# Optimization experiments

Measured on AMD Instinct MI355X. Metric: run time of the kernel, lower is better.

The kernel has to match this reference:

```python
import jax, jax.numpy as jnp
import numpy as np

S, D, H, DK, DV = 4096, 1024, 16, 64, 64


def setup_inputs() -> dict:
    key = jax.random.key(0)
    ks = jax.random.split(key, 6)
    x = jax.random.normal(ks[0], (S, D), dtype=jnp.float32)
    # per-head projection weights, stacked over heads; scaled for numerical sanity
    Wq = jax.random.normal(ks[1], (H, D, DK), dtype=jnp.float32) / np.sqrt(D)
    Wk = jax.random.normal(ks[2], (H, D, DK), dtype=jnp.float32) / np.sqrt(D)
    Wv = jax.random.normal(ks[3], (H, D, DV), dtype=jnp.float32) / np.sqrt(D)
    Wc = jax.random.normal(ks[4], (H * DV, D), dtype=jnp.float32) / np.sqrt(H * DV)
    bc = jnp.zeros((D,), dtype=jnp.float32)
    return {"x": x, "Wq": Wq, "Wk": Wk, "Wv": Wv, "Wc": Wc, "bc": bc}


def reference(x, Wq, Wk, Wv, Wc, bc):
    # Per-head projections (original loops over heads with separate Linears;
    # stacking over h is the same math, vectorized).
    q = jnp.einsum("sd,hdk->hsk", x, Wq)   # [H,S,DK]
    k = jnp.einsum("sd,hdk->hsk", x, Wk)   # [H,S,DK]
    v = jnp.einsum("sd,hdv->hsv", x, Wv)   # [H,S,DV]
    scores = jnp.einsum("hsk,htk->hst", q, k) / jnp.sqrt(jnp.asarray(DK, x.dtype))
    probs = jax.nn.softmax(scores, axis=-1)  # softmax over last dim, per row
    o = jnp.einsum("hst,htv->hsv", probs, v)  # [H,S,DV]
    cat = jnp.transpose(o, (1, 0, 2)).reshape(S, H * DV)  # concat heads on last dim
    return cat @ Wc + bc  # output projection with bias
```

## Files before the change

kernel.cpp:

```cpp
#include <hip/hip_runtime.h>
#include <hip/hip_bf16.h>

#define S_ 4096
#define D_ 1024
#define H_ 16
#define DK_ 64
#define DV_ 64

typedef short bf16x8 __attribute__((ext_vector_type(8)));
typedef float floatx4 __attribute__((ext_vector_type(4)));
using bf16 = __hip_bfloat16;

#define MFMA16(a, b, c) __builtin_amdgcn_mfma_f32_16x16x32_bf16(a, b, c, 0, 0, 0)

__device__ __forceinline__ void stage16(const void* g, void* l) {
    __builtin_amdgcn_global_load_lds(
        (const __attribute__((address_space(1))) void*)g,
        (__attribute__((address_space(3))) void*)l, 16, 0, 0);
}

__device__ __forceinline__ bf16x8 ldsfrag(const bf16* base, int row, int chunk) {
    return *(const bf16x8*)(base + row * 64 + ((chunk ^ (row & 7)) << 3));
}

__global__ __launch_bounds__(256)
void cvt_x(const float* __restrict__ x, bf16* __restrict__ xb)
{
    int i = (blockIdx.x * 256 + threadIdx.x) * 8;
    float4 a = *(const float4*)(x + i);
    float4 b = *(const float4*)(x + i + 4);
    union { bf16x8 v; bf16 e[8]; } u;
    u.e[0] = __float2bfloat16(a.x); u.e[1] = __float2bfloat16(a.y);
    u.e[2] = __float2bfloat16(a.z); u.e[3] = __float2bfloat16(a.w);
    u.e[4] = __float2bfloat16(b.x); u.e[5] = __float2bfloat16(b.y);
    u.e[6] = __float2bfloat16(b.z); u.e[7] = __float2bfloat16(b.w);
    *(bf16x8*)(xb + i) = u.v;
}

__global__ __launch_bounds__(256)
void transpose_cvt(const float* __restrict__ src, bf16* __restrict__ dst,
                   int R, int C, long srcMatStride, long dstMatStride, float scale)
{
    const float* s = src + (size_t)blockIdx.z * srcMatStride;
    bf16* d = dst + (size_t)blockIdx.z * dstMatStride;
    int r0 = blockIdx.x * 64, c0 = blockIdx.y * 64;
    __shared__ float ls[64][65];
    int t = threadIdx.x;
    {
        int r = t >> 2, cseg = (t & 3) * 16;
        const float* sp = s + (size_t)(r0 + r) * C + c0 + cseg;
        #pragma unroll
        for (int i = 0; i < 16; i += 4) {
            float4 v = *(const float4*)(sp + i);
            ls[r][cseg + i + 0] = v.x; ls[r][cseg + i + 1] = v.y;
            ls[r][cseg + i + 2] = v.z; ls[r][cseg + i + 3] = v.w;
        }
    }
    __syncthreads();
    {
        int c = t >> 2, rseg = (t & 3) * 16;
        bf16* dp = d + (size_t)(c0 + c) * R + r0 + rseg;
        #pragma unroll
        for (int i = 0; i < 16; i++) dp[i] = __float2bfloat16(ls[rseg + i][c] * scale);
    }
}

__global__ __launch_bounds__(256)
void qkv_gemm(const bf16* __restrict__ xb, const bf16* __restrict__ Wt,
              bf16* __restrict__ Qb, bf16* __restrict__ Kb, bf16* __restrict__ Vtb)
{
    const int m0 = blockIdx.x * 128;
    const int h  = blockIdx.y;
    __shared__ __align__(16) bf16 xa[2][128 * 64];
    __shared__ __align__(16) bf16 wb[2][192 * 64];

    const int t = threadIdx.x, lane = t & 63, w = t >> 6;
    const int l15 = lane & 15, quad = lane >> 4;

    auto stage_x = [&](int buf, int kk) {
        #pragma unroll
        for (int j = 0; j < 4; j++) {
            int c = (j * 4 + w) * 64 + lane;
            int row = c >> 3, ch = (c & 7) ^ (row & 7);
            stage16((const char*)(xb + (size_t)(m0 + row) * D_ + kk) + ch * 16,
                    (char*)&xa[buf][0] + (j * 4 + w) * 1024);
        }
    };
    auto stage_w = [&](int buf, int kk) {
        #pragma unroll
        for (int j = 0; j < 6; j++) {
            int c = (j * 4 + w) * 64 + lane;
            int row = c >> 3, ch = (c & 7) ^ (row & 7);
            const bf16* g = Wt + (size_t)(row >> 6) * (H_ * 64 * 1024)
                               + (size_t)h * (64 * 1024)
                               + (size_t)(row & 63) * 1024 + kk;
            stage16((const char*)g + ch * 16, (char*)&wb[buf][0] + (j * 4 + w) * 1024);
        }
    };

    const floatx4 fz = {0.f, 0.f, 0.f, 0.f};
    floatx4 acc[2][12];
    #pragma unroll
    for (int mt = 0; mt < 2; mt++)
        #pragma unroll
        for (int nt = 0; nt < 12; nt++) acc[mt][nt] = fz;

    stage_x(0, 0); stage_w(0, 0);
    for (int kt = 0; kt < 16; kt++) {
        int cur = kt & 1;
        __syncthreads();
        if (kt < 15) { stage_x(cur ^ 1, (kt + 1) * 64); stage_w(cur ^ 1, (kt + 1) * 64); }
        #pragma unroll
        for (int ks = 0; ks < 2; ks++) {
            bf16x8 a0 = ldsfrag(&xa[cur][0], w * 32 + l15,      ks * 4 + quad);
            bf16x8 a1 = ldsfrag(&xa[cur][0], w * 32 + 16 + l15, ks * 4 + quad);
            #pragma unroll
            for (int nt = 0; nt < 12; nt++) {
                bf16x8 b = ldsfrag(&wb[cur][0], nt * 16 + l15, ks * 4 + quad);
                acc[0][nt] = MFMA16(a0, b, acc[0][nt]);
                acc[1][nt] = MFMA16(a1, b, acc[1][nt]);
            }
        }
    }

    #pragma unroll
    for (int nt = 0; nt < 12; nt++) {
        int which = nt >> 2;
        int col = (nt & 3) * 16 + l15;
        #pragma unroll
        for (int mt = 0; mt < 2; mt++)
            #pragma unroll
            for (int r = 0; r < 4; r++) {
                int s = m0 + w * 32 + mt * 16 + quad * 4 + r;
                bf16 val = __float2bfloat16(acc[mt][nt][r]);
                if (which == 0)      Qb[((size_t)h * S_ + s) * 64 + col] = val;
                else if (which == 1) Kb[((size_t)h * S_ + s) * 64 + col] = val;
                else                 Vtb[((size_t)h * 64 + col) * S_ + s] = val;
            }
    }
}

__global__ __launch_bounds__(256)
void attn(const bf16* __restrict__ Qb, const bf16* __restrict__ Kb,
          const bf16* __restrict__ Vtb, bf16* __restrict__ Cat)
{
    const int m0 = blockIdx.x * 128;
    const int h  = blockIdx.y;
    __shared__ __align__(16) bf16 ka[2][64 * 64];
    __shared__ __align__(16) bf16 vt[2][64 * 64];
    __shared__ __align__(16) bf16 pl[128 * 72];

    const int t = threadIdx.x, lane = t & 63, w = t >> 6;
    const int l15 = lane & 15, quad = lane >> 4;

    auto stage_kv = [&](int buf, int key0) {
        const char* kg = (const char*)(Kb + ((size_t)h * S_ + key0) * 64);
        #pragma unroll
        for (int j = 0; j < 2; j++) {
            int c = (j * 4 + w) * 64 + lane;
            int row = c >> 3, ch = (c & 7) ^ (row & 7);
            stage16(kg + row * 128 + ch * 16, (char*)&ka[buf][0] + (j * 4 + w) * 1024);
        }
        const char* vg = (const char*)(Vtb + (size_t)h * 64 * S_ + key0);
        #pragma unroll
        for (int j = 0; j < 2; j++) {
            int c = (j * 4 + w) * 64 + lane;
            int row = c >> 3, ch = (c & 7) ^ (row & 7);
            stage16(vg + (size_t)row * (S_ * 2) + ch * 16, (char*)&vt[buf][0] + (j * 4 + w) * 1024);
        }
    };

    {
        const char* qg = (const char*)(Qb + ((size_t)h * S_ + m0) * 64);
        #pragma unroll
        for (int j = 0; j < 4; j++) {
            int c = (j * 4 + w) * 64 + lane;
            int row = c >> 3, ch = (c & 7) ^ (row & 7);
            stage16(qg + row * 128 + ch * 16, (char*)pl + (j * 4 + w) * 1024);
        }
    }
    stage_kv(0, 0);
    __syncthreads();

    bf16x8 qf[2][2];
    #pragma unroll
    for (int mt = 0; mt < 2; mt++)
        #pragma unroll
        for (int ks = 0; ks < 2; ks++)
            qf[mt][ks] = ldsfrag((const bf16*)pl, w * 32 + mt * 16 + l15, ks * 4 + quad);
    __syncthreads();

    const floatx4 fz = {0.f, 0.f, 0.f, 0.f};
    floatx4 acc[2][4];
    float rs[2][4];
    #pragma unroll
    for (int mt = 0; mt < 2; mt++) {
        #pragma unroll
        for (int nt = 0; nt < 4; nt++) acc[mt][nt] = fz;
        #pragma unroll
        for (int r = 0; r < 4; r++) rs[mt][r] = 0.f;
    }

    for (int kt = 0; kt < S_ / 64; kt++) {
        const int cur = kt & 1;
        if (kt + 1 < S_ / 64) stage_kv(cur ^ 1, (kt + 1) * 64);

        floatx4 sc[2][4];
        #pragma unroll
        for (int mt = 0; mt < 2; mt++)
            #pragma unroll
            for (int nt = 0; nt < 4; nt++) sc[mt][nt] = fz;
        #pragma unroll
        for (int ks = 0; ks < 2; ks++) {
            #pragma unroll
            for (int nt = 0; nt < 4; nt++) {
                bf16x8 b = ldsfrag(&ka[cur][0], nt * 16 + l15, ks * 4 + quad);
                sc[0][nt] = MFMA16(qf[0][ks], b, sc[0][nt]);
                sc[1][nt] = MFMA16(qf[1][ks], b, sc[1][nt]);
            }
        }

        #pragma unroll
        for (int mt = 0; mt < 2; mt++)
            #pragma unroll
            for (int nt = 0; nt < 4; nt++)
                #pragma unroll
                for (int r = 0; r < 4; r++) {
                    float p = __expf(sc[mt][nt][r]);
                    rs[mt][r] += p;
                    pl[(w * 32 + mt * 16 + quad * 4 + r) * 72 + nt * 16 + l15] =
                        __float2bfloat16(p);
                }
        asm volatile("s_waitcnt lgkmcnt(0)" ::: "memory");

        #pragma unroll
        for (int ks = 0; ks < 2; ks++) {
            bf16x8 a0 = *(const bf16x8*)(pl + (w * 32 + l15) * 72 + ks * 32 + quad * 8);
            bf16x8 a1 = *(const bf16x8*)(pl + (w * 32 + 16 + l15) * 72 + ks * 32 + quad * 8);
            #pragma unroll
            for (int nt = 0; nt < 4; nt++) {
                bf16x8 b = ldsfrag(&vt[cur][0], nt * 16 + l15, ks * 4 + quad);
                acc[0][nt] = MFMA16(a0, b, acc[0][nt]);
                acc[1][nt] = MFMA16(a1, b, acc[1][nt]);
            }
        }
        __syncthreads();
    }

    #pragma unroll
    for (int mt = 0; mt < 2; mt++)
        #pragma unroll
        for (int r = 0; r < 4; r++) {
            float s_ = rs[mt][r];
            s_ += __shfl_xor(s_, 1, 16);
            s_ += __shfl_xor(s_, 2, 16);
            s_ += __shfl_xor(s_, 4, 16);
            s_ += __shfl_xor(s_, 8, 16);
            float inv = 1.0f / s_;
            int srow = m0 + w * 32 + mt * 16 + quad * 4 + r;
            #pragma unroll
            for (int nt = 0; nt < 4; nt++)
                Cat[(size_t)srow * (H_ * DV_) + h * 64 + nt * 16 + l15] =
                    __float2bfloat16(acc[mt][nt][r] * inv);
        }
}

__global__ __launch_bounds__(256)
void out_proj(const bf16* __restrict__ Cat, const bf16* __restrict__ Wct,
              const float* __restrict__ bc, float* __restrict__ out)
{
    const int m0 = blockIdx.x * 128;
    const int n0 = blockIdx.y * 128;
    __shared__ __align__(16) bf16 ca[2][128 * 64];
    __shared__ __align__(16) bf16 wb[2][128 * 64];

    const int t = threadIdx.x, lane = t & 63, w = t >> 6;
    const int l15 = lane & 15, quad = lane >> 4;

    auto stage_a = [&](int buf, int kk) {
        #pragma unroll
        for (int j = 0; j < 4; j++) {
            int c = (j * 4 + w) * 64 + lane;
            int row = c >> 3, ch = (c & 7) ^ (row & 7);
            stage16((const char*)(Cat + (size_t)(m0 + row) * D_ + kk) + ch * 16,
                    (char*)&ca[buf][0] + (j * 4 + w) * 1024);
        }
    };
    auto stage_b = [&](int buf, int kk) {
        #pragma unroll
        for (int j = 0; j < 4; j++) {
            int c = (j * 4 + w) * 64 + lane;
            int row = c >> 3, ch = (c & 7) ^ (row & 7);
            stage16((const char*)(Wct + (size_t)(n0 + row) * D_ + kk) + ch * 16,
                    (char*)&wb[buf][0] + (j * 4 + w) * 1024);
        }
    };

    const floatx4 fz = {0.f, 0.f, 0.f, 0.f};
    floatx4 acc[2][8];
    #pragma unroll
    for (int mt = 0; mt < 2; mt++)
        #pragma unroll
        for (int nt = 0; nt < 8; nt++) acc[mt][nt] = fz;

    stage_a(0, 0); stage_b(0, 0);
    for (int kt = 0; kt < 16; kt++) {
        int cur = kt & 1;
        __syncthreads();
        if (kt < 15) { stage_a(cur ^ 1, (kt + 1) * 64); stage_b(cur ^ 1, (kt + 1) * 64); }
        #pragma unroll
        for (int ks = 0; ks < 2; ks++) {
            bf16x8 a0 = ldsfrag(&ca[cur][0], w * 32 + l15,      ks * 4 + quad);
            bf16x8 a1 = ldsfrag(&ca[cur][0], w * 32 + 16 + l15, ks * 4 + quad);
            #pragma unroll
            for (int nt = 0; nt < 8; nt++) {
                bf16x8 b = ldsfrag(&wb[cur][0], nt * 16 + l15, ks * 4 + quad);
                acc[0][nt] = MFMA16(a0, b, acc[0][nt]);
                acc[1][nt] = MFMA16(a1, b, acc[1][nt]);
            }
        }
    }

    #pragma unroll
    for (int nt = 0; nt < 8; nt++) {
        int col = n0 + nt * 16 + l15;
        float bias = bc[col];
        #pragma unroll
        for (int mt = 0; mt < 2; mt++)
            #pragma unroll
            for (int r = 0; r < 4; r++) {
                int row = m0 + w * 32 + mt * 16 + quad * 4 + r;
                out[(size_t)row * D_ + col] = acc[mt][nt][r] + bias;
            }
    }
}

extern "C" void kernel_launch(void* const* d_in, const int* in_sizes, int n_in,
                              void* d_out, int out_size, void* d_ws, size_t ws_size,
                              hipStream_t stream)
{
    const float* x  = (const float*)d_in[0];
    const float* Wq = (const float*)d_in[1];
    const float* Wk = (const float*)d_in[2];
    const float* Wv = (const float*)d_in[3];
    const float* Wc = (const float*)d_in[4];
    const float* bc = (const float*)d_in[5];
    float* out = (float*)d_out;

    bf16* xb  = (bf16*)d_ws;
    bf16* Cat = xb;
    bf16* Wt  = xb  + (size_t)S_ * D_;
    bf16* Wct = Wt  + (size_t)3 * H_ * 64 * D_;
    bf16* Qb  = Wct + (size_t)D_ * H_ * DV_;
    bf16* Kb  = Qb  + (size_t)H_ * S_ * 64;
    bf16* Vtb = Kb  + (size_t)H_ * S_ * 64;

    const long wMat = (long)D_ * 64;
    const long wHead = (long)H_ * 64 * D_;

    cvt_x<<<dim3(S_ * D_ / (256 * 8)), 256, 0, stream>>>(x, xb);
    transpose_cvt<<<dim3(16, 1, 16), 256, 0, stream>>>(Wq, Wt,             1024, 64, wMat, wMat, 0.125f);
    transpose_cvt<<<dim3(16, 1, 16), 256, 0, stream>>>(Wk, Wt + wHead,     1024, 64, wMat, wMat, 1.0f);
    transpose_cvt<<<dim3(16, 1, 16), 256, 0, stream>>>(Wv, Wt + 2 * wHead, 1024, 64, wMat, wMat, 1.0f);
    transpose_cvt<<<dim3(16, 16, 1), 256, 0, stream>>>(Wc, Wct,            1024, 1024, 0, 0, 1.0f);

    qkv_gemm<<<dim3(S_ / 128, H_), 256, 0, stream>>>(xb, Wt, Qb, Kb, Vtb);
    attn<<<dim3(S_ / 128, H_), 256, 0, stream>>>(Qb, Kb, Vtb, Cat);
    out_proj<<<dim3(S_ / 128, D_ / 128), 256, 0, stream>>>(Cat, Wct, bc, out);
}
```

Measured before the change: 271.8 us.

## Split attention over key halves, retile QKV GEMM, fold log2e into Wq, merge weight transposes

The attention kernel gains a split-K path that processes half the keys per block, writes fp32 partial outputs and row sums, and merges them in a new combine kernel. This doubles the number of attention blocks for better occupancy, at the cost of extra partial-output traffic and one more launch. The path runs only when the workspace is large enough. Other changes: log2(e) is folded into the Wq scale so exp2 can replace expf, the QK product is computed transposed with Q fragments read directly from global memory, and the QKV GEMM is retiled into 128-wide N tiles over 3072 columns. The out projection uses 64-wide N tiles and the weight transposes are merged into fewer launches.

```diff
diff --git a/kernel.cpp b/kernel.cpp
--- a/kernel.cpp
+++ b/kernel.cpp
@@ -13,6 +13,12 @@
 
 #define MFMA16(a, b, c) __builtin_amdgcn_mfma_f32_16x16x32_bf16(a, b, c, 0, 0, 0)
 
+#if __has_builtin(__builtin_amdgcn_exp2f)
+#define EXP2(x) __builtin_amdgcn_exp2f(x)
+#else
+#define EXP2(x) exp2f(x)
+#endif
+
 __device__ __forceinline__ void stage16(const void* g, void* l) {
     __builtin_amdgcn_global_load_lds(
         (const __attribute__((address_space(1))) void*)g,
@@ -20,7 +26,11 @@
 }
 
 __device__ __forceinline__ bf16x8 ldsfrag(const bf16* base, int row, int chunk) {
-    return *(const bf16x8*)(base + row * 64 + ((chunk ^ (row & 7)) << 3));
+    return *(const bf16x8*)(base + row * 64 + (((chunk ^ (row & 7))) << 3));
+}
+
+__device__ __forceinline__ unsigned short bfbits(float f) {
+    union { bf16 h; unsigned short u; } c; c.h = __float2bfloat16(f); return c.u;
 }
 
 __global__ __launch_bounds__(256)
@@ -29,26 +39,52 @@
     int i = (blockIdx.x * 256 + threadIdx.x) * 8;
     float4 a = *(const float4*)(x + i);
     float4 b = *(const float4*)(x + i + 4);
-    union { bf16x8 v; bf16 e[8]; } u;
-    u.e[0] = __float2bfloat16(a.x); u.e[1] = __float2bfloat16(a.y);
-    u.e[2] = __float2bfloat16(a.z); u.e[3] = __float2bfloat16(a.w);
-    u.e[4] = __float2bfloat16(b.x); u.e[5] = __float2bfloat16(b.y);
-    u.e[6] = __float2bfloat16(b.z); u.e[7] = __float2bfloat16(b.w);
-    *(bf16x8*)(xb + i) = u.v;
-}
-
-__global__ __launch_bounds__(256)
-void transpose_cvt(const float* __restrict__ src, bf16* __restrict__ dst,
-                   int R, int C, long srcMatStride, long dstMatStride, float scale)
-{
-    const float* s = src + (size_t)blockIdx.z * srcMatStride;
-    bf16* d = dst + (size_t)blockIdx.z * dstMatStride;
+    ushort4 lo, hi;
+    lo.x = bfbits(a.x); lo.y = bfbits(a.y); lo.z = bfbits(a.z); lo.w = bfbits(a.w);
+    hi.x = bfbits(b.x); hi.y = bfbits(b.y); hi.z = bfbits(b.z); hi.w = bfbits(b.w);
+    *(ushort4*)(xb + i) = lo;
+    *(ushort4*)(xb + i + 4) = hi;
+}
+
+__global__ __launch_bounds__(256)
+void tr_qkv(const float* __restrict__ Wq, const float* __restrict__ Wk,
+            const float* __restrict__ Wv, bf16* __restrict__ Wt)
+{
+    const int z = blockIdx.z, which = z >> 4, h = z & 15;
+    const float* s = (which == 0 ? Wq : which == 1 ? Wk : Wv) + (size_t)h * D_ * 64;
+    bf16* d = Wt + ((size_t)which * 1024 + h * 64) * D_;
+    const float scale = (which == 0) ? 0.125f * 1.44269504088896340736f : 1.0f;
+    const int r0 = blockIdx.x * 64;
+    __shared__ float ls[64][65];
+    int t = threadIdx.x;
+    {
+        int r = t >> 2, cseg = (t & 3) * 16;
+        const float* sp = s + (size_t)(r0 + r) * 64 + cseg;
+        #pragma unroll
+        for (int i = 0; i < 16; i += 4) {
+            float4 v = *(const float4*)(sp + i);
+            ls[r][cseg + i + 0] = v.x; ls[r][cseg + i + 1] = v.y;
+            ls[r][cseg + i + 2] = v.z; ls[r][cseg + i + 3] = v.w;
+        }
+    }
+    __syncthreads();
+    {
+        int c = t >> 2, rseg = (t & 3) * 16;
+        bf16* dp = d + (size_t)c * D_ + r0 + rseg;
+        #pragma unroll
+        for (int i = 0; i < 16; i++) dp[i] = __float2bfloat16(ls[rseg + i][c] * scale);
+    }
+}
+
+__global__ __launch_bounds__(256)
+void tr_wc(const float* __restrict__ src, bf16* __restrict__ dst)
+{
     int r0 = blockIdx.x * 64, c0 = blockIdx.y * 64;
     __shared__ float ls[64][65];
     int t = threadIdx.x;
     {
         int r = t >> 2, cseg = (t & 3) * 16;
-        const float* sp = s + (size_t)(r0 + r) * C + c0 + cseg;
+        const float* sp = src + (size_t)(r0 + r) * D_ + c0 + cseg;
         #pragma unroll
         for (int i = 0; i < 16; i += 4) {
             float4 v = *(const float4*)(sp + i);
@@ -59,9 +95,9 @@
     __syncthreads();
     {
         int c = t >> 2, rseg = (t & 3) * 16;
-        bf16* dp = d + (size_t)(c0 + c) * R + r0 + rseg;
-        #pragma unroll
-        for (int i = 0; i < 16; i++) dp[i] = __float2bfloat16(ls[rseg + i][c] * scale);
+        bf16* dp = dst + (size_t)(c0 + c) * D_ + r0 + rseg;
+        #pragma unroll
+        for (int i = 0; i < 16; i++) dp[i] = __float2bfloat16(ls[rseg + i][c]);
     }
 }
 
@@ -70,14 +106,14 @@
               bf16* __restrict__ Qb, bf16* __restrict__ Kb, bf16* __restrict__ Vtb)
 {
     const int m0 = blockIdx.x * 128;
-    const int h  = blockIdx.y;
+    const int n0 = blockIdx.y * 128;
     __shared__ __align__(16) bf16 xa[2][128 * 64];
-    __shared__ __align__(16) bf16 wb[2][192 * 64];
+    __shared__ __align__(16) bf16 wb2[2][128 * 64];
 
     const int t = threadIdx.x, lane = t & 63, w = t >> 6;
     const int l15 = lane & 15, quad = lane >> 4;
 
-    auto stage_x = [&](int buf, int kk) {
+    auto stage_a = [&](int buf, int kk) {
         #pragma unroll
         for (int j = 0; j < 4; j++) {
             int c = (j * 4 + w) * 64 + lane;
@@ -86,213 +122,13 @@
                     (char*)&xa[buf][0] + (j * 4 + w) * 1024);
         }
     };
-    auto stage_w = [&](int buf, int kk) {
-        #pragma unroll
-        for (int j = 0; j < 6; j++) {
-            int c = (j * 4 + w) * 64 + lane;
-            int row = c >> 3, ch = (c & 7) ^ (row & 7);
-            const bf16* g = Wt + (size_t)(row >> 6) * (H_ * 64 * 1024)
-                               + (size_t)h * (64 * 1024)
-                               + (size_t)(row & 63) * 1024 + kk;
-            stage16((const char*)g + ch * 16, (char*)&wb[buf][0] + (j * 4 + w) * 1024);
-        }
-    };
-
-    const floatx4 fz = {0.f, 0.f, 0.f, 0.f};
-    floatx4 acc[2][12];
-    #pragma unroll
-    for (int mt = 0; mt < 2; mt++)
-        #pragma unroll
-        for (int nt = 0; nt < 12; nt++) acc[mt][nt] = fz;
-
-    stage_x(0, 0); stage_w(0, 0);
-    for (int kt = 0; kt < 16; kt++) {
-        int cur = kt & 1;
-        __syncthreads();
-        if (kt < 15) { stage_x(cur ^ 1, (kt + 1) * 64); stage_w(cur ^ 1, (kt + 1) * 64); }
-        #pragma unroll
-        for (int ks = 0; ks < 2; ks++) {
-            bf16x8 a0 = ldsfrag(&xa[cur][0], w * 32 + l15,      ks * 4 + quad);
-            bf16x8 a1 = ldsfrag(&xa[cur][0], w * 32 + 16 + l15, ks * 4 + quad);
-            #pragma unroll
-            for (int nt = 0; nt < 12; nt++) {
-                bf16x8 b = ldsfrag(&wb[cur][0], nt * 16 + l15, ks * 4 + quad);
-                acc[0][nt] = MFMA16(a0, b, acc[0][nt]);
-                acc[1][nt] = MFMA16(a1, b, acc[1][nt]);
-            }
-        }
-    }
-
-    #pragma unroll
-    for (int nt = 0; nt < 12; nt++) {
-        int which = nt >> 2;
-        int col = (nt & 3) * 16 + l15;
-        #pragma unroll
-        for (int mt = 0; mt < 2; mt++)
-            #pragma unroll
-            for (int r = 0; r < 4; r++) {
-                int s = m0 + w * 32 + mt * 16 + quad * 4 + r;
-                bf16 val = __float2bfloat16(acc[mt][nt][r]);
-                if (which == 0)      Qb[((size_t)h * S_ + s) * 64 + col] = val;
-                else if (which == 1) Kb[((size_t)h * S_ + s) * 64 + col] = val;
-                else                 Vtb[((size_t)h * 64 + col) * S_ + s] = val;
-            }
-    }
-}
-
-__global__ __launch_bounds__(256)
-void attn(const bf16* __restrict__ Qb, const bf16* __restrict__ Kb,
-          const bf16* __restrict__ Vtb, bf16* __restrict__ Cat)
-{
-    const int m0 = blockIdx.x * 128;
-    const int h  = blockIdx.y;
-    __shared__ __align__(16) bf16 ka[2][64 * 64];
-    __shared__ __align__(16) bf16 vt[2][64 * 64];
-    __shared__ __align__(16) bf16 pl[128 * 72];
-
-    const int t = threadIdx.x, lane = t & 63, w = t >> 6;
-    const int l15 = lane & 15, quad = lane >> 4;
-
-    auto stage_kv = [&](int buf, int key0) {
-        const char* kg = (const char*)(Kb + ((size_t)h * S_ + key0) * 64);
-        #pragma unroll
-        for (int j = 0; j < 2; j++) {
-            int c = (j * 4 + w) * 64 + lane;
-            int row = c >> 3, ch = (c & 7) ^ (row & 7);
-            stage16(kg + row * 128 + ch * 16, (char*)&ka[buf][0] + (j * 4 + w) * 1024);
-        }
-        const char* vg = (const char*)(Vtb + (size_t)h * 64 * S_ + key0);
-        #pragma unroll
-        for (int j = 0; j < 2; j++) {
-            int c = (j * 4 + w) * 64 + lane;
-            int row = c >> 3, ch = (c & 7) ^ (row & 7);
-            stage16(vg + (size_t)row * (S_ * 2) + ch * 16, (char*)&vt[buf][0] + (j * 4 + w) * 1024);
-        }
-    };
-
-    {
-        const char* qg = (const char*)(Qb + ((size_t)h * S_ + m0) * 64);
+    auto stage_b = [&](int buf, int kk) {
         #pragma unroll
         for (int j = 0; j < 4; j++) {
             int c = (j * 4 + w) * 64 + lane;
             int row = c >> 3, ch = (c & 7) ^ (row & 7);
-            stage16(qg + row * 128 + ch * 16, (char*)pl + (j * 4 + w) * 1024);
-        }
-    }
-    stage_kv(0, 0);
-    __syncthreads();
-
-    bf16x8 qf[2][2];
-    #pragma unroll
-    for (int mt = 0; mt < 2; mt++)
-        #pragma unroll
-        for (int ks = 0; ks < 2; ks++)
-            qf[mt][ks] = ldsfrag((const bf16*)pl, w * 32 + mt * 16 + l15, ks * 4 + quad);
-    __syncthreads();
-
-    const floatx4 fz = {0.f, 0.f, 0.f, 0.f};
-    floatx4 acc[2][4];
-    float rs[2][4];
-    #pragma unroll
-    for (int mt = 0; mt < 2; mt++) {
-        #pragma unroll
-        for (int nt = 0; nt < 4; nt++) acc[mt][nt] = fz;
-        #pragma unroll
-        for (int r = 0; r < 4; r++) rs[mt][r] = 0.f;
-    }
-
-    for (int kt = 0; kt < S_ / 64; kt++) {
-        const int cur = kt & 1;
-        if (kt + 1 < S_ / 64) stage_kv(cur ^ 1, (kt + 1) * 64);
-
-        floatx4 sc[2][4];
-        #pragma unroll
-        for (int mt = 0; mt < 2; mt++)
-            #pragma unroll
-            for (int nt = 0; nt < 4; nt++) sc[mt][nt] = fz;
-        #pragma unroll
-        for (int ks = 0; ks < 2; ks++) {
-            #pragma unroll
-            for (int nt = 0; nt < 4; nt++) {
-                bf16x8 b = ldsfrag(&ka[cur][0], nt * 16 + l15, ks * 4 + quad);
-                sc[0][nt] = MFMA16(qf[0][ks], b, sc[0][nt]);
-                sc[1][nt] = MFMA16(qf[1][ks], b, sc[1][nt]);
-            }
-        }
-
-        #pragma unroll
-        for (int mt = 0; mt < 2; mt++)
-            #pragma unroll
-            for (int nt = 0; nt < 4; nt++)
-                #pragma unroll
-                for (int r = 0; r < 4; r++) {
-                    float p = __expf(sc[mt][nt][r]);
-                    rs[mt][r] += p;
-                    pl[(w * 32 + mt * 16 + quad * 4 + r) * 72 + nt * 16 + l15] =
-                        __float2bfloat16(p);
-                }
-        asm volatile("s_waitcnt lgkmcnt(0)" ::: "memory");
-
-        #pragma unroll
-        for (int ks = 0; ks < 2; ks++) {
-            bf16x8 a0 = *(const bf16x8*)(pl + (w * 32 + l15) * 72 + ks * 32 + quad * 8);
-            bf16x8 a1 = *(const bf16x8*)(pl + (w * 32 + 16 + l15) * 72 + ks * 32 + quad * 8);
-            #pragma unroll
-            for (int nt = 0; nt < 4; nt++) {
-                bf16x8 b = ldsfrag(&vt[cur][0], nt * 16 + l15, ks * 4 + quad);
-                acc[0][nt] = MFMA16(a0, b, acc[0][nt]);
-                acc[1][nt] = MFMA16(a1, b, acc[1][nt]);
-            }
-        }
-        __syncthreads();
-    }
-
-    #pragma unroll
-    for (int mt = 0; mt < 2; mt++)
-        #pragma unroll
-        for (int r = 0; r < 4; r++) {
-            float s_ = rs[mt][r];
-            s_ += __shfl_xor(s_, 1, 16);
-            s_ += __shfl_xor(s_, 2, 16);
-            s_ += __shfl_xor(s_, 4, 16);
-            s_ += __shfl_xor(s_, 8, 16);
-            float inv = 1.0f / s_;
-            int srow = m0 + w * 32 + mt * 16 + quad * 4 + r;
-            #pragma unroll
-            for (int nt = 0; nt < 4; nt++)
-                Cat[(size_t)srow * (H_ * DV_) + h * 64 + nt * 16 + l15] =
-                    __float2bfloat16(acc[mt][nt][r] * inv);
-        }
-}
-
-__global__ __launch_bounds__(256)
-void out_proj(const bf16* __restrict__ Cat, const bf16* __restrict__ Wct,
-              const float* __restrict__ bc, float* __restrict__ out)
-{
-    const int m0 = blockIdx.x * 128;
-    const int n0 = blockIdx.y * 128;
-    __shared__ __align__(16) bf16 ca[2][128 * 64];
-    __shared__ __align__(16) bf16 wb[2][128 * 64];
-
-    const int t = threadIdx.x, lane = t & 63, w = t >> 6;
-    const int l15 = lane & 15, quad = lane >> 4;
-
-    auto stage_a = [&](int buf, int kk) {
-        #pragma unroll
-        for (int j = 0; j < 4; j++) {
-            int c = (j * 4 + w) * 64 + lane;
-            int row = c >> 3, ch = (c & 7) ^ (row & 7);
-            stage16((const char*)(Cat + (size_t)(m0 + row) * D_ + kk) + ch * 16,
-                    (char*)&ca[buf][0] + (j * 4 + w) * 1024);
-        }
-    };
-    auto stage_b = [&](int buf, int kk) {
-        #pragma unroll
-        for (int j = 0; j < 4; j++) {
-            int c = (j * 4 + w) * 64 + lane;
-            int row = c >> 3, ch = (c & 7) ^ (row & 7);
-            stage16((const char*)(Wct + (size_t)(n0 + row) * D_ + kk) + ch * 16,
-                    (char*)&wb[buf][0] + (j * 4 + w) * 1024);
+            stage16((const char*)(Wt + (size_t)(n0 + row) * D_ + kk) + ch * 16,
+                    (char*)&wb2[buf][0] + (j * 4 + w) * 1024);
         }
     };
 
@@ -310,11 +146,249 @@
         if (kt < 15) { stage_a(cur ^ 1, (kt + 1) * 64); stage_b(cur ^ 1, (kt + 1) * 64); }
         #pragma unroll
         for (int ks = 0; ks < 2; ks++) {
+            bf16x8 a0 = ldsfrag(&xa[cur][0], w * 32 + l15,      ks * 4 + quad);
+            bf16x8 a1 = ldsfrag(&xa[cur][0], w * 32 + 16 + l15, ks * 4 + quad);
+            #pragma unroll
+            for (int nt = 0; nt < 8; nt++) {
+                bf16x8 b = ldsfrag(&wb2[cur][0], nt * 16 + l15, ks * 4 + quad);
+                acc[0][nt] = MFMA16(a0, b, acc[0][nt]);
+                acc[1][nt] = MFMA16(a1, b, acc[1][nt]);
+            }
+        }
+    }
+
+    const int which = n0 >> 10;
+    #pragma unroll
+    for (int nt = 0; nt < 8; nt++) {
+        int n = n0 + nt * 16 + l15;
+        int hh = (n >> 6) & 15, col = n & 63;
+        #pragma unroll
+        for (int mt = 0; mt < 2; mt++)
+            #pragma unroll
+            for (int r = 0; r < 4; r++) {
+                int s = m0 + w * 32 + mt * 16 + quad * 4 + r;
+                bf16 val = __float2bfloat16(acc[mt][nt][r]);
+                if (which == 0)      Qb[((size_t)hh * S_ + s) * 64 + col] = val;
+                else if (which == 1) Kb[((size_t)hh * S_ + s) * 64 + col] = val;
+                else                 Vtb[((size_t)hh * 64 + col) * S_ + s] = val;
+            }
+    }
+}
+
+template<int NKT, bool FULL>
+__global__ __launch_bounds__(256)
+void attn(const bf16* __restrict__ Qb, const bf16* __restrict__ Kb,
+          const bf16* __restrict__ Vtb, bf16* __restrict__ Cat,
+          float* __restrict__ Opart, float* __restrict__ lpart)
+{
+    const int m0 = blockIdx.x * 128;
+    const int h  = blockIdx.y;
+    const int half = blockIdx.z;
+    const int keybase = half * (NKT * 64);
+
+    __shared__ __align__(16) bf16 ka[2][64 * 64];
+    __shared__ __align__(16) bf16 vt[2][64 * 64];
+    __shared__ __align__(16) bf16 pl[128 * 64];
+    __shared__ float lsum[128];
+
+    const int t = threadIdx.x, lane = t & 63, w = t >> 6;
+    const int l15 = lane & 15, quad = lane >> 4;
+
+    auto stage_kv = [&](int buf, int key0) {
+        const char* kg = (const char*)(Kb + ((size_t)h * S_ + key0) * 64);
+        #pragma unroll
+        for (int j = 0; j < 2; j++) {
+            int c = (j * 4 + w) * 64 + lane;
+            int row = c >> 3, ch = (c & 7) ^ (row & 7);
+            stage16(kg + row * 128 + ch * 16, (char*)&ka[buf][0] + (j * 4 + w) * 1024);
+        }
+        const char* vg = (const char*)(Vtb + (size_t)h * 64 * S_ + key0);
+        #pragma unroll
+        for (int j = 0; j < 2; j++) {
+            int c = (j * 4 + w) * 64 + lane;
+            int row = c >> 3, ch = (c & 7) ^ (row & 7);
+            stage16(vg + (size_t)row * (S_ * 2) + ch * 16, (char*)&vt[buf][0] + (j * 4 + w) * 1024);
+        }
+    };
+
+    bf16x8 qf[2][2];
+    #pragma unroll
+    for (int nq = 0; nq < 2; nq++)
+        #pragma unroll
+        for (int ks = 0; ks < 2; ks++)
+            qf[nq][ks] = *(const bf16x8*)(Qb +
+                ((size_t)h * S_ + m0 + w * 32 + nq * 16 + l15) * 64 + ks * 32 + quad * 8);
+
+    const floatx4 fz = {0.f, 0.f, 0.f, 0.f};
+    floatx4 acc[2][4];
+    float rs[2] = {0.f, 0.f};
+    #pragma unroll
+    for (int mt = 0; mt < 2; mt++)
+        #pragma unroll
+        for (int nt = 0; nt < 4; nt++) acc[mt][nt] = fz;
+
+    stage_kv(0, keybase);
+    __syncthreads();
+
+    for (int kt = 0; kt < NKT; kt++) {
+        const int cur = kt & 1;
+        if (kt + 1 < NKT) stage_kv(cur ^ 1, keybase + (kt + 1) * 64);
+
+        floatx4 sc[4][2];
+        #pragma unroll
+        for (int mk = 0; mk < 4; mk++)
+            #pragma unroll
+            for (int nq = 0; nq < 2; nq++) sc[mk][nq] = fz;
+        #pragma unroll
+        for (int ks = 0; ks < 2; ks++) {
+            bf16x8 af[4];
+            #pragma unroll
+            for (int mk = 0; mk < 4; mk++)
+                af[mk] = ldsfrag(&ka[cur][0], mk * 16 + l15, ks * 4 + quad);
+            #pragma unroll
+            for (int mk = 0; mk < 4; mk++)
+                #pragma unroll
+                for (int nq = 0; nq < 2; nq++)
+                    sc[mk][nq] = MFMA16(af[mk], qf[nq][ks], sc[mk][nq]);
+        }
+
+        #pragma unroll
+        for (int mk = 0; mk < 4; mk++)
+            #pragma unroll
+            for (int nq = 0; nq < 2; nq++) {
+                float p0 = EXP2(sc[mk][nq][0]);
+                float p1 = EXP2(sc[mk][nq][1]);
+                float p2 = EXP2(sc[mk][nq][2]);
+                float p3 = EXP2(sc[mk][nq][3]);
+                rs[nq] += (p0 + p1) + (p2 + p3);
+                ushort4 pw;
+                pw.x = bfbits(p0); pw.y = bfbits(p1); pw.z = bfbits(p2); pw.w = bfbits(p3);
+                int q = w * 32 + nq * 16 + l15;
+                int ch = 2 * mk + (quad >> 1);
+                *(ushort4*)((char*)pl + q * 128 + ((ch ^ (q & 7)) << 4) + (quad & 1) * 8) = pw;
+            }
+        asm volatile("s_waitcnt lgkmcnt(0)" ::: "memory");
+
+        #pragma unroll
+        for (int ks = 0; ks < 2; ks++) {
+            bf16x8 a0 = ldsfrag(pl, w * 32 + l15,      ks * 4 + quad);
+            bf16x8 a1 = ldsfrag(pl, w * 32 + 16 + l15, ks * 4 + quad);
+            #pragma unroll
+            for (int nt = 0; nt < 4; nt++) {
+                bf16x8 b = ldsfrag(&vt[cur][0], nt * 16 + l15, ks * 4 + quad);
+                acc[0][nt] = MFMA16(a0, b, acc[0][nt]);
+                acc[1][nt] = MFMA16(a1, b, acc[1][nt]);
+            }
+        }
+        __syncthreads();
+    }
+
+    #pragma unroll
+    for (int nq = 0; nq < 2; nq++) {
+        rs[nq] += __shfl_xor(rs[nq], 16);
+        rs[nq] += __shfl_xor(rs[nq], 32);
+        if (quad == 0) lsum[w * 32 + nq * 16 + l15] = rs[nq];
+    }
+    asm volatile("s_waitcnt lgkmcnt(0)" ::: "memory");
+
+    if (FULL) {
+        #pragma unroll
+        for (int mt = 0; mt < 2; mt++)
+            #pragma unroll
+            for (int r = 0; r < 4; r++) {
+                int rl = w * 32 + mt * 16 + quad * 4 + r;
+                float inv = 1.0f / lsum[rl];
+                #pragma unroll
+                for (int nt = 0; nt < 4; nt++)
+                    Cat[(size_t)(m0 + rl) * (H_ * DV_) + h * 64 + nt * 16 + l15] =
+                        __float2bfloat16(acc[mt][nt][r] * inv);
+            }
+    } else {
+        const size_t plane = (size_t)(half * H_ + h) * S_;
+        #pragma unroll
+        for (int mt = 0; mt < 2; mt++)
+            #pragma unroll
+            for (int r = 0; r < 4; r++) {
+                int rl = w * 32 + mt * 16 + quad * 4 + r;
+                #pragma unroll
+                for (int nt = 0; nt < 4; nt++)
+                    Opart[(plane + m0 + rl) * 64 + nt * 16 + l15] = acc[mt][nt][r];
+            }
+        #pragma unroll
+        for (int nq = 0; nq < 2; nq++)
+            if (quad == 0)
+                lpart[plane + m0 + w * 32 + nq * 16 + l15] = rs[nq];
+    }
+}
+
+__global__ __launch_bounds__(256)
+void combine(const float* __restrict__ Opart, const float* __restrict__ lpart,
+             bf16* __restrict__ Cat)
+{
+    const int h = blockIdx.y;
+    const int off = blockIdx.x * 1024 + threadIdx.x * 4;
+    const int s = off >> 6, dv = off & 63;
+    float4 o0 = *(const float4*)(Opart + (size_t)h * S_ * 64 + off);
+    float4 o1 = *(const float4*)(Opart + (size_t)(H_ + h) * S_ * 64 + off);
+    float inv = 1.0f / (lpart[(size_t)h * S_ + s] + lpart[(size_t)(H_ + h) * S_ + s]);
+    ushort4 o;
+    o.x = bfbits((o0.x + o1.x) * inv);
+    o.y = bfbits((o0.y + o1.y) * inv);
+    o.z = bfbits((o0.z + o1.z) * inv);
+    o.w = bfbits((o0.w + o1.w) * inv);
+    *(ushort4*)(Cat + (size_t)s * (H_ * DV_) + h * 64 + dv) = o;
+}
+
+__global__ __launch_bounds__(256)
+void out_proj(const bf16* __restrict__ Cat, const bf16* __restrict__ Wct,
+              const float* __restrict__ bc, float* __restrict__ out)
+{
+    const int m0 = blockIdx.x * 128;
+    const int n0 = blockIdx.y * 64;
+    __shared__ __align__(16) bf16 ca[2][128 * 64];
+    __shared__ __align__(16) bf16 wb2[2][64 * 64];
+
+    const int t = threadIdx.x, lane = t & 63, w = t >> 6;
+    const int l15 = lane & 15, quad = lane >> 4;
+
+    auto stage_a = [&](int buf, int kk) {
+        #pragma unroll
+        for (int j = 0; j < 4; j++) {
+            int c = (j * 4 + w) * 64 + lane;
+            int row = c >> 3, ch = (c & 7) ^ (row & 7);
+            stage16((const char*)(Cat + (size_t)(m0 + row) * D_ + kk) + ch * 16,
+                    (char*)&ca[buf][0] + (j * 4 + w) * 1024);
+        }
+    };
+    auto stage_b = [&](int buf, int kk) {
+        #pragma unroll
+        for (int j = 0; j < 2; j++) {
+            int c = (j * 4 + w) * 64 + lane;
+            int row = c >> 3, ch = (c & 7) ^ (row & 7);
+            stage16((const char*)(Wct + (size_t)(n0 + row) * D_ + kk) + ch * 16,
+                    (char*)&wb2[buf][0] + (j * 4 + w) * 1024);
+        }
+    };
+
+    const floatx4 fz = {0.f, 0.f, 0.f, 0.f};
+    floatx4 acc[2][4];
+    #pragma unroll
+    for (int mt = 0; mt < 2; mt++)
+        #pragma unroll
+        for (int nt = 0; nt < 4; nt++) acc[mt][nt] = fz;
+
+    stage_a(0, 0); stage_b(0, 0);
+    for (int kt = 0; kt < 16; kt++) {
+        int cur = kt & 1;
+        __syncthreads();
+        if (kt < 15) { stage_a(cur ^ 1, (kt + 1) * 64); stage_b(cur ^ 1, (kt + 1) * 64); }
+        #pragma unroll
+        for (int ks = 0; ks < 2; ks++) {
             bf16x8 a0 = ldsfrag(&ca[cur][0], w * 32 + l15,      ks * 4 + quad);
             bf16x8 a1 = ldsfrag(&ca[cur][0], w * 32 + 16 + l15, ks * 4 + quad);
             #pragma unroll
-            for (int nt = 0; nt < 8; nt++) {
-                bf16x8 b = ldsfrag(&wb[cur][0], nt * 16 + l15, ks * 4 + quad);
+            for (int nt = 0; nt < 4; nt++) {
+                bf16x8 b = ldsfrag(&wb2[cur][0], nt * 16 + l15, ks * 4 + quad);
                 acc[0][nt] = MFMA16(a0, b, acc[0][nt]);
                 acc[1][nt] = MFMA16(a1, b, acc[1][nt]);
             }
@@ -322,7 +396,7 @@
     }
 
     #pragma unroll
-    for (int nt = 0; nt < 8; nt++) {
+    for (int nt = 0; nt < 4; nt++) {
         int col = n0 + nt * 16 + l15;
         float bias = bc[col];
         #pragma unroll
@@ -354,17 +428,26 @@
     bf16* Qb  = Wct + (size_t)D_ * H_ * DV_;
     bf16* Kb  = Qb  + (size_t)H_ * S_ * 64;
     bf16* Vtb = Kb  + (size_t)H_ * S_ * 64;
-
-    const long wMat = (long)D_ * 64;
-    const long wHead = (long)H_ * 64 * D_;
+    float* Opart = (float*)(Vtb + (size_t)H_ * 64 * S_);
+    float* lpart = Opart + (size_t)2 * H_ * S_ * 64;
+
+    const size_t need_split = (size_t)((char*)(lpart + (size_t)2 * H_ * S_) - (char*)d_ws);
+    const bool split = ws_size >= need_split;
 
     cvt_x<<<dim3(S_ * D_ / (256 * 8)), 256, 0, stream>>>(x, xb);
-    transpose_cvt<<<dim3(16, 1, 16), 256, 0, stream>>>(Wq, Wt,             1024, 64, wMat, wMat, 0.125f);
-    transpose_cvt<<<dim3(16, 1, 16), 256, 0, stream>>>(Wk, Wt + wHead,     1024, 64, wMat, wMat, 1.0f);
-    transpose_cvt<<<dim3(16, 1, 16), 256, 0, stream>>>(Wv, Wt + 2 * wHead, 1024, 64, wMat, wMat, 1.0f);
-    transpose_cvt<<<dim3(16, 16, 1), 256, 0, stream>>>(Wc, Wct,            1024, 1024, 0, 0, 1.0f);
-
-    qkv_gemm<<<dim3(S_ / 128, H_), 256, 0, stream>>>(xb, Wt, Qb, Kb, Vtb);
-    attn<<<dim3(S_ / 128, H_), 256, 0, stream>>>(Qb, Kb, Vtb, Cat);
-    out_proj<<<dim3(S_ / 128, D_ / 128), 256, 0, stream>>>(Cat, Wct, bc, out);
-}
+    tr_qkv<<<dim3(16, 1, 48), 256, 0, stream>>>(Wq, Wk, Wv, Wt);
+    tr_wc<<<dim3(16, 16), 256, 0, stream>>>(Wc, Wct);
+
+    qkv_gemm<<<dim3(S_ / 128, 3072 / 128), 256, 0, stream>>>(xb, Wt, Qb, Kb, Vtb);
+
+    if (split) {
+        attn<32, false><<<dim3(S_ / 128, H_, 2), 256, 0, stream>>>(
+            Qb, Kb, Vtb, Cat, Opart, lpart);
+        combine<<<dim3(S_ * 64 / 1024, H_), 256, 0, stream>>>(Opart, lpart, Cat);
+    } else {
+        attn<64, true><<<dim3(S_ / 128, H_, 1), 256, 0, stream>>>(
+            Qb, Kb, Vtb, Cat, Opart, lpart);
+    }
+
+    out_proj<<<dim3(S_ / 128, D_ / 64), 256, 0, stream>>>(Cat, Wct, bc, out);
+}
```

New measurement: 269.7 us. No clear change (-0.8%).
